# Performance work log

Measured on AMD Instinct MI355X. Metric: run time of the kernel, lower is better.

The kernel has to match this reference:

```python
import jax, jax.numpy as jnp
import numpy as np

B, N, F, H, L = 8, 512, 32, 64, 2

def setup_inputs() -> dict:
    key = jax.random.key(0)
    ks = jax.random.split(key, 16)
    s = lambda fan_in: 1.0 / np.sqrt(fan_in)
    return {
        "x": jax.random.normal(ks[0], (B, N, F), dtype=jnp.float32),
        # node encoder: Linear(F, H), stored as [in, out]
        "W_enc": jax.random.uniform(ks[1], (F, H), minval=-s(F), maxval=s(F)),
        "b_enc": jax.random.uniform(ks[2], (H,), minval=-s(F), maxval=s(F)),
        # edge MLP: Linear(2H, H) then Linear(H, 1)
        "W_e1": jax.random.uniform(ks[3], (2 * H, H), minval=-s(2 * H), maxval=s(2 * H)),
        "b_e1": jax.random.uniform(ks[4], (H,), minval=-s(2 * H), maxval=s(2 * H)),
        "W_e2": jax.random.uniform(ks[5], (H,), minval=-s(H), maxval=s(H)),
        "b_e2": jax.random.uniform(ks[6], (), minval=-s(H), maxval=s(H)),
        # per-layer message Linear(H, H)
        "W_msg": jax.random.uniform(ks[7], (L, H, H), minval=-s(H), maxval=s(H)),
        "b_msg": jax.random.uniform(ks[8], (L, H), minval=-s(H), maxval=s(H)),
        # per-layer GRUCell(H, H): gates ordered [r, z, n], stored as [in, 3H]
        "W_ih": jax.random.uniform(ks[9], (L, H, 3 * H), minval=-s(H), maxval=s(H)),
        "b_ih": jax.random.uniform(ks[10], (L, 3 * H), minval=-s(H), maxval=s(H)),
        "W_hh": jax.random.uniform(ks[11], (L, H, 3 * H), minval=-s(H), maxval=s(H)),
        "b_hh": jax.random.uniform(ks[12], (L, 3 * H), minval=-s(H), maxval=s(H)),
        # output Linear(H, 1)
        "W_out": jax.random.uniform(ks[13], (H, 1), minval=-s(H), maxval=s(H)),
        "b_out": jax.random.uniform(ks[14], (1,), minval=-s(H), maxval=s(H)),
    }

def reference(x, W_enc, b_enc, W_e1, b_e1, W_e2, b_e2, W_msg, b_msg,
              W_ih, b_ih, W_hh, b_hh, W_out, b_out):
    # Node encoding (dropout is eval-mode identity)
    h = jax.nn.relu(x @ W_enc + b_enc)  # [B, N, H]

    # Edge MLP on pairwise concat [h_i, h_j]: split W_e1 so we never build the 2H concat
    Wa, Wb = W_e1[:H], W_e1[H:]
    zi = h @ Wa                           # contribution of h_i, [B, N, H]
    zj = h @ Wb                           # contribution of h_j, [B, N, H]
    e = jax.nn.relu(zi[:, :, None, :] + zj[:, None, :, :] + b_e1)  # [B, N, N, H]
    logits = jnp.einsum('bijh,h->bij', e, W_e2) + b_e2             # [B, N, N]

    eye = jnp.eye(logits.shape[-1], dtype=bool)
    logits = jnp.where(eye[None], -jnp.inf, logits)
    adj = jax.nn.softmax(logits, axis=-1)
    adj = jnp.nan_to_num(adj, nan=0.0, posinf=0.0, neginf=0.0)

    for l in range(L):
        m = jnp.einsum('bij,bjh->bih', adj, h)             # message aggregation
        m = jax.nn.relu(m @ W_msg[l] + b_msg[l])
        # GRUCell update (gates [r, z, n])
        gi = m @ W_ih[l] + b_ih[l]
        gh = h @ W_hh[l] + b_hh[l]
        ir, iz, inn = jnp.split(gi, 3, axis=-1)
        hr, hz, hn = jnp.split(gh, 3, axis=-1)
        r = jax.nn.sigmoid(ir + hr)
        z = jax.nn.sigmoid(iz + hz)
        n = jnp.tanh(inn + r * hn)
        h = (1.0 - z) * n + z * h

    graph_emb = jnp.mean(h, axis=1)       # [B, H]
    return graph_emb @ W_out + b_out      # [B, 1]
```

## Files before the change

kernel.cpp:

```cpp
#include <hip/hip_runtime.h>
#include <math.h>

#define BB 8
#define NN 512
#define FF 32
#define HH 64
#define NEG_BIG (-1.0e30f)

__device__ __forceinline__ float lane_bcast(float v, int l) {
    return __int_as_float(__builtin_amdgcn_readlane(__float_as_int(v), l));
}

__global__ __launch_bounds__(256) void encode_kernel(
    const float* __restrict__ x, const float* __restrict__ W_enc,
    const float* __restrict__ b_enc, const float* __restrict__ W_e1,
    const float* __restrict__ b_e1,
    float* __restrict__ h, float* __restrict__ zi, float* __restrict__ zjT2)
{
    const int t = threadIdx.x;
    const int hh = t & 63;
    const int qu = __builtin_amdgcn_readfirstlane(t >> 6);
    const int gR = blockIdx.x * 4 + qu;

    const float xv = x[gR * FF + (hh & 31)];
    float acc = b_enc[hh];
#pragma unroll 8
    for (int k = 0; k < FF; ++k)
        acc = fmaf(lane_bcast(xv, k), W_enc[k * HH + hh], acc);
    const float hval = fmaxf(acc, 0.f);
    h[gR * HH + hh] = hval;

    float z1 = b_e1[hh], z2 = 0.f;
#pragma unroll 8
    for (int k = 0; k < HH; ++k) {
        const float hk = lane_bcast(hval, k);
        z1 = fmaf(hk, W_e1[k * HH + hh], z1);
        z2 = fmaf(hk, W_e1[(HH + k) * HH + hh], z2);
    }
    zi[gR * HH + hh] = z1;
    const int b = gR >> 9, n = gR & (NN - 1);
    zjT2[(((size_t)b * 32 + (hh >> 1)) * NN + n) * 2 + (hh & 1)] = z2;
}

__global__ __launch_bounds__(512, 8) void adj_kernel(
    const float* __restrict__ zi, const float* __restrict__ zjT2,
    const float* __restrict__ We2, const float* __restrict__ be2,
    const float* __restrict__ b_out,
    float* __restrict__ adjw, float* __restrict__ out)
{
    const int b  = blockIdx.x >> 7;
    const int i0 = (blockIdx.x & 127) << 2;
    const int t  = threadIdx.x;
    const int tj = t & 63;
    const int w  = __builtin_amdgcn_readfirstlane(t >> 6);
    const int gR0 = b * NN + i0;
    const int j   = 64 * w + tj;

    __shared__ float redm[8][4], reds[8][4];

    if (blockIdx.x < BB && t == 0) out[blockIdx.x] = b_out[0];

    const float2* zi2 = (const float2*)(zi + (size_t)gR0 * HH);
    const float2* we2 = (const float2*)We2;
    const float2* zt2 = (const float2*)zjT2 + (size_t)b * 32 * NN + j;

    float2 a2[4];
#pragma unroll
    for (int r = 0; r < 4; ++r) a2[r] = make_float2(0.f, 0.f);
#pragma unroll 8
    for (int k2 = 0; k2 < 32; ++k2) {
        const float2 z = zt2[(size_t)k2 * NN];
        const float2 wk = we2[k2];
#pragma unroll
        for (int r = 0; r < 4; ++r) {
            const float2 zv = zi2[r * 32 + k2];
            a2[r].x = fmaf(fmaxf(zv.x + z.x, 0.f), wk.x, a2[r].x);
            a2[r].y = fmaf(fmaxf(zv.y + z.y, 0.f), wk.y, a2[r].y);
        }
    }
    const float bias2 = be2[0];
    float acc[4];
#pragma unroll
    for (int r = 0; r < 4; ++r) {
        acc[r] = a2[r].x + a2[r].y + bias2;
        if (j == i0 + r) acc[r] = NEG_BIG;
    }

#pragma unroll
    for (int r = 0; r < 4; ++r) {
        float m = acc[r];
#pragma unroll
        for (int off = 32; off >= 1; off >>= 1)
            m = fmaxf(m, __shfl_xor(m, off));
        if (tj == 0) redm[w][r] = m;
    }
    __syncthreads();
    float M[4];
#pragma unroll
    for (int r = 0; r < 4; ++r) {
        float m = redm[0][r];
#pragma unroll
        for (int p = 1; p < 8; ++p) m = fmaxf(m, redm[p][r]);
        M[r] = m;
    }
    float e[4];
#pragma unroll
    for (int r = 0; r < 4; ++r) {
        e[r] = __expf(acc[r] - M[r]);
        float s = e[r];
#pragma unroll
        for (int off = 32; off >= 1; off >>= 1) s += __shfl_xor(s, off);
        if (tj == 0) reds[w][r] = s;
    }
    __syncthreads();
#pragma unroll
    for (int r = 0; r < 4; ++r) {
        float s = reds[0][r];
#pragma unroll
        for (int p = 1; p < 8; ++p) s += reds[p][r];
        adjw[(size_t)(gR0 + r) * NN + j] = e[r] * (1.0f / s);
    }
}

template <int LAST>
__global__ __launch_bounds__(512, 8) void layer_kernel(
    const float* __restrict__ adjr, const float* __restrict__ h_in,
    const float* __restrict__ Wmsg, const float* __restrict__ bmsg,
    const float* __restrict__ Wih, const float* __restrict__ bih,
    const float* __restrict__ Whh, const float* __restrict__ bhh,
    const float* __restrict__ Wout,
    float* __restrict__ h_out, float* __restrict__ out)
{
    const int b  = blockIdx.x >> 7;
    const int i0 = (blockIdx.x & 127) << 2;
    const int t  = threadIdx.x;
    const int tj = t & 63;
    const int w  = __builtin_amdgcn_readfirstlane(t >> 6);
    const int gR0 = b * NN + i0;

    __shared__ float smem[3168];
    __shared__ float mml[4][66];
    __shared__ float hol[4][66];
#define RED(p, r, c)        smem[(((p) * 4) + (r)) * 66 + (c)]
#define GP(h2, k2, r, g, c) smem[(((((h2) * 2 + (k2)) * 4 + (r)) * 3 + (g)) * 66) + (c)]

    if (w < 4) hol[w][tj] = h_in[(size_t)(gR0 + w) * HH + tj];

    {
        const float* hq = h_in + ((size_t)b * NN + 64 * w) * HH + tj;
        const float* a0 = adjr + (size_t)(gR0 + 0) * NN + 64 * w;
        const float* a1 = adjr + (size_t)(gR0 + 1) * NN + 64 * w;
        const float* a2 = adjr + (size_t)(gR0 + 2) * NN + 64 * w;
        const float* a3 = adjr + (size_t)(gR0 + 3) * NN + 64 * w;
        float mac[4] = {0.f, 0.f, 0.f, 0.f};
#pragma unroll 8
        for (int jj = 0; jj < 64; ++jj) {
            const float hv = hq[(size_t)jj * HH];
            mac[0] = fmaf(a0[jj], hv, mac[0]);
            mac[1] = fmaf(a1[jj], hv, mac[1]);
            mac[2] = fmaf(a2[jj], hv, mac[2]);
            mac[3] = fmaf(a3[jj], hv, mac[3]);
        }
#pragma unroll
        for (int r = 0; r < 4; ++r) RED(w, r, tj) = mac[r];
    }
    __syncthreads();

    if (w < 4) {
        float m = RED(0, w, tj);
#pragma unroll
        for (int p = 1; p < 8; ++p) m += RED(p, w, tj);
        float mmv = bmsg[tj];
#pragma unroll 8
        for (int k = 0; k < HH; ++k)
            mmv = fmaf(lane_bcast(m, k), Wmsg[k * HH + tj], mmv);
        mml[w][tj] = fmaxf(mmv, 0.f);
    }
    __syncthreads();

    {
        const int half = w >> 2, kh = (w >> 1) & 1, rq = w & 1;
        const float* Wg = half ? Whh : Wih;
        const float* bg = half ? bhh : bih;
        float sreg[2];
#pragma unroll
        for (int r = 0; r < 2; ++r)
            sreg[r] = half ? hol[rq * 2 + r][tj] : mml[rq * 2 + r][tj];
        float g0[2], g1[2], g2[2];
#pragma unroll
        for (int r = 0; r < 2; ++r) {
            g0[r] = kh ? 0.f : bg[tj];
            g1[r] = kh ? 0.f : bg[64 + tj];
            g2[r] = kh ? 0.f : bg[128 + tj];
        }
        const int k0 = kh * 32;
#pragma unroll 4
        for (int kk = 0; kk < 32; ++kk) {
            const float* wk = Wg + (size_t)(k0 + kk) * 192;
            const float w0 = wk[tj], w1 = wk[64 + tj], w2 = wk[128 + tj];
#pragma unroll
            for (int r = 0; r < 2; ++r) {
                const float s = lane_bcast(sreg[r], k0 + kk);
                g0[r] = fmaf(s, w0, g0[r]);
                g1[r] = fmaf(s, w1, g1[r]);
                g2[r] = fmaf(s, w2, g2[r]);
            }
        }
#pragma unroll
        for (int r = 0; r < 2; ++r) {
            GP(half, kh, rq * 2 + r, 0, tj) = g0[r];
            GP(half, kh, rq * 2 + r, 1, tj) = g1[r];
            GP(half, kh, rq * 2 + r, 2, tj) = g2[r];
        }
    }
    __syncthreads();

    float hnew = 0.f;
    if (w < 4) {
        const float ir  = GP(0, 0, w, 0, tj) + GP(0, 1, w, 0, tj);
        const float iz  = GP(0, 0, w, 1, tj) + GP(0, 1, w, 1, tj);
        const float inn = GP(0, 0, w, 2, tj) + GP(0, 1, w, 2, tj);
        const float hr  = GP(1, 0, w, 0, tj) + GP(1, 1, w, 0, tj);
        const float hz  = GP(1, 0, w, 1, tj) + GP(1, 1, w, 1, tj);
        const float hn  = GP(1, 0, w, 2, tj) + GP(1, 1, w, 2, tj);
        const float rg = 1.f / (1.f + __expf(-(ir + hr)));
        const float zg = 1.f / (1.f + __expf(-(iz + hz)));
        const float ng = tanhf(inn + rg * hn);
        hnew = (1.f - zg) * ng + zg * hol[w][tj];
        h_out[(size_t)(gR0 + w) * HH + tj] = hnew;
    }

    if (LAST) {
        __syncthreads();
        if (w < 4) mml[w][tj] = hnew;
        __syncthreads();
        if (w == 0) {
            float v = (mml[0][tj] + mml[1][tj] + mml[2][tj] + mml[3][tj])
                      * (1.0f / NN) * Wout[tj];
#pragma unroll
            for (int off = 32; off >= 1; off >>= 1) v += __shfl_xor(v, off);
            if (tj == 0) atomicAdd(out + b, v);
        }
    }
#undef RED
#undef GP
}

extern "C" void kernel_launch(void* const* d_in, const int* in_sizes, int n_in,
                              void* d_out, int out_size, void* d_ws, size_t ws_size,
                              hipStream_t stream)
{
    const float* x     = (const float*)d_in[0];
    const float* W_enc = (const float*)d_in[1];
    const float* b_enc = (const float*)d_in[2];
    const float* W_e1  = (const float*)d_in[3];
    const float* b_e1  = (const float*)d_in[4];
    const float* W_e2  = (const float*)d_in[5];
    const float* b_e2  = (const float*)d_in[6];
    const float* W_msg = (const float*)d_in[7];
    const float* b_msg = (const float*)d_in[8];
    const float* W_ih  = (const float*)d_in[9];
    const float* b_ih  = (const float*)d_in[10];
    const float* W_hh  = (const float*)d_in[11];
    const float* b_hh  = (const float*)d_in[12];
    const float* W_out = (const float*)d_in[13];
    const float* b_out = (const float*)d_in[14];
    float* out = (float*)d_out;

    float* ws   = (float*)d_ws;
    float* h0   = ws;
    float* h1   = h0 + BB * NN * HH;
    float* zi   = h1 + BB * NN * HH;
    float* zjT2 = zi + BB * NN * HH;
    float* adjw = zjT2 + BB * NN * HH;

    encode_kernel<<<BB * NN / 4, 256, 0, stream>>>(
        x, W_enc, b_enc, W_e1, b_e1, h0, zi, zjT2);

    adj_kernel<<<BB * (NN / 4), 512, 0, stream>>>(
        zi, zjT2, W_e2, b_e2, b_out, adjw, out);

    layer_kernel<0><<<BB * (NN / 4), 512, 0, stream>>>(
        adjw, h0, W_msg, b_msg, W_ih, b_ih, W_hh, b_hh, W_out, h1, out);
    layer_kernel<1><<<BB * (NN / 4), 512, 0, stream>>>(
        adjw, h1, W_msg + HH * HH, b_msg + HH,
        W_ih + HH * 3 * HH, b_ih + 3 * HH, W_hh + HH * 3 * HH, b_hh + 3 * HH,
        W_out, h0, out);
}
```

Before: 72.19 us.

## Overlap hidden-state GRU gate matmul with message aggregation across waves

The layer kernel now splits its 8 waves by role. Waves 0-3 do the adjacency-times-h aggregation over 128 columns each, instead of all 8 waves doing 64 columns. At the same time waves 4-7 compute the W_hh gate projections for the 4 rows, which do not depend on the messages. This removes W_hh work from the later gate phase, which then only computes the input-side W_ih gates across all waves. The aggregation phase has half as many waves doing longer serial loops, which could lengthen the critical path.

```diff
diff --git a/kernel.cpp b/kernel.cpp
--- a/kernel.cpp
+++ b/kernel.cpp
@@ -138,23 +138,20 @@
     const int w  = __builtin_amdgcn_readfirstlane(t >> 6);
     const int gR0 = b * NN + i0;
 
-    __shared__ float smem[3168];
+    __shared__ float RED[4][4][66];
+    __shared__ float GHL[4][3][66];
+    __shared__ float GPI[2][4][3][66];
     __shared__ float mml[4][66];
-    __shared__ float hol[4][66];
-#define RED(p, r, c)        smem[(((p) * 4) + (r)) * 66 + (c)]
-#define GP(h2, k2, r, g, c) smem[(((((h2) * 2 + (k2)) * 4 + (r)) * 3 + (g)) * 66) + (c)]
-
-    if (w < 4) hol[w][tj] = h_in[(size_t)(gR0 + w) * HH + tj];
-
-    {
-        const float* hq = h_in + ((size_t)b * NN + 64 * w) * HH + tj;
-        const float* a0 = adjr + (size_t)(gR0 + 0) * NN + 64 * w;
-        const float* a1 = adjr + (size_t)(gR0 + 1) * NN + 64 * w;
-        const float* a2 = adjr + (size_t)(gR0 + 2) * NN + 64 * w;
-        const float* a3 = adjr + (size_t)(gR0 + 3) * NN + 64 * w;
+
+    if (w < 4) {
+        const float* hq = h_in + ((size_t)b * NN + 128 * w) * HH + tj;
+        const float* a0 = adjr + (size_t)(gR0 + 0) * NN + 128 * w;
+        const float* a1 = adjr + (size_t)(gR0 + 1) * NN + 128 * w;
+        const float* a2 = adjr + (size_t)(gR0 + 2) * NN + 128 * w;
+        const float* a3 = adjr + (size_t)(gR0 + 3) * NN + 128 * w;
         float mac[4] = {0.f, 0.f, 0.f, 0.f};
 #pragma unroll 8
-        for (int jj = 0; jj < 64; ++jj) {
+        for (int jj = 0; jj < 128; ++jj) {
             const float hv = hq[(size_t)jj * HH];
             mac[0] = fmaf(a0[jj], hv, mac[0]);
             mac[1] = fmaf(a1[jj], hv, mac[1]);
@@ -162,14 +159,28 @@
             mac[3] = fmaf(a3[jj], hv, mac[3]);
         }
 #pragma unroll
-        for (int r = 0; r < 4; ++r) RED(w, r, tj) = mac[r];
+        for (int r = 0; r < 4; ++r) RED[w][r][tj] = mac[r];
+    } else {
+        const int rr = w - 4;
+        const float hreg = h_in[(size_t)(gR0 + rr) * HH + tj];
+        float g3 = bhh[tj], g4 = bhh[64 + tj], g5 = bhh[128 + tj];
+#pragma unroll 4
+        for (int k = 0; k < HH; ++k) {
+            const float sh = lane_bcast(hreg, k);
+            const float* wh = Whh + (size_t)k * 192;
+            g3 = fmaf(sh, wh[tj], g3);
+            g4 = fmaf(sh, wh[64 + tj], g4);
+            g5 = fmaf(sh, wh[128 + tj], g5);
+        }
+        GHL[rr][0][tj] = g3;
+        GHL[rr][1][tj] = g4;
+        GHL[rr][2][tj] = g5;
     }
     __syncthreads();
 
     if (w < 4) {
-        float m = RED(0, w, tj);
-#pragma unroll
-        for (int p = 1; p < 8; ++p) m += RED(p, w, tj);
+        const float m = RED[0][w][tj] + RED[1][w][tj]
+                      + RED[2][w][tj] + RED[3][w][tj];
         float mmv = bmsg[tj];
 #pragma unroll 8
         for (int k = 0; k < HH; ++k)
@@ -179,54 +190,39 @@
     __syncthreads();
 
     {
-        const int half = w >> 2, kh = (w >> 1) & 1, rq = w & 1;
-        const float* Wg = half ? Whh : Wih;
-        const float* bg = half ? bhh : bih;
-        float sreg[2];
-#pragma unroll
-        for (int r = 0; r < 2; ++r)
-            sreg[r] = half ? hol[rq * 2 + r][tj] : mml[rq * 2 + r][tj];
-        float g0[2], g1[2], g2[2];
-#pragma unroll
-        for (int r = 0; r < 2; ++r) {
-            g0[r] = kh ? 0.f : bg[tj];
-            g1[r] = kh ? 0.f : bg[64 + tj];
-            g2[r] = kh ? 0.f : bg[128 + tj];
-        }
+        const int kh = w >> 2, r = w & 3;
+        const float srcv = mml[r][tj];
+        float g0 = kh ? 0.f : bih[tj];
+        float g1 = kh ? 0.f : bih[64 + tj];
+        float g2 = kh ? 0.f : bih[128 + tj];
         const int k0 = kh * 32;
 #pragma unroll 4
         for (int kk = 0; kk < 32; ++kk) {
-            const float* wk = Wg + (size_t)(k0 + kk) * 192;
-            const float w0 = wk[tj], w1 = wk[64 + tj], w2 = wk[128 + tj];
-#pragma unroll
-            for (int r = 0; r < 2; ++r) {
-                const float s = lane_bcast(sreg[r], k0 + kk);
-                g0[r] = fmaf(s, w0, g0[r]);
-                g1[r] = fmaf(s, w1, g1[r]);
-                g2[r] = fmaf(s, w2, g2[r]);
-            }
-        }
-#pragma unroll
-        for (int r = 0; r < 2; ++r) {
-            GP(half, kh, rq * 2 + r, 0, tj) = g0[r];
-            GP(half, kh, rq * 2 + r, 1, tj) = g1[r];
-            GP(half, kh, rq * 2 + r, 2, tj) = g2[r];
-        }
+            const float* wi = Wih + (size_t)(k0 + kk) * 192;
+            const float s = lane_bcast(srcv, k0 + kk);
+            g0 = fmaf(s, wi[tj], g0);
+            g1 = fmaf(s, wi[64 + tj], g1);
+            g2 = fmaf(s, wi[128 + tj], g2);
+        }
+        GPI[kh][r][0][tj] = g0;
+        GPI[kh][r][1][tj] = g1;
+        GPI[kh][r][2][tj] = g2;
     }
     __syncthreads();
 
     float hnew = 0.f;
     if (w < 4) {
-        const float ir  = GP(0, 0, w, 0, tj) + GP(0, 1, w, 0, tj);
-        const float iz  = GP(0, 0, w, 1, tj) + GP(0, 1, w, 1, tj);
-        const float inn = GP(0, 0, w, 2, tj) + GP(0, 1, w, 2, tj);
-        const float hr  = GP(1, 0, w, 0, tj) + GP(1, 1, w, 0, tj);
-        const float hz  = GP(1, 0, w, 1, tj) + GP(1, 1, w, 1, tj);
-        const float hn  = GP(1, 0, w, 2, tj) + GP(1, 1, w, 2, tj);
+        const float hprev = h_in[(size_t)(gR0 + w) * HH + tj];
+        const float ir  = GPI[0][w][0][tj] + GPI[1][w][0][tj];
+        const float iz  = GPI[0][w][1][tj] + GPI[1][w][1][tj];
+        const float inn = GPI[0][w][2][tj] + GPI[1][w][2][tj];
+        const float hr  = GHL[w][0][tj];
+        const float hz  = GHL[w][1][tj];
+        const float hn  = GHL[w][2][tj];
         const float rg = 1.f / (1.f + __expf(-(ir + hr)));
         const float zg = 1.f / (1.f + __expf(-(iz + hz)));
         const float ng = tanhf(inn + rg * hn);
-        hnew = (1.f - zg) * ng + zg * hol[w][tj];
+        hnew = (1.f - zg) * ng + zg * hprev;
         h_out[(size_t)(gR0 + w) * HH + tj] = hnew;
     }
 
@@ -242,8 +238,6 @@
             if (tj == 0) atomicAdd(out + b, v);
         }
     }
-#undef RED
-#undef GP
 }
 
 extern "C" void kernel_launch(void* const* d_in, const int* in_sizes, int n_in,
```

New measurement: 78.96 us. +9.4%, slower.
